# Performance work log

Measured on AMD Instinct MI355X. Metric: run time of the kernel, lower is better.

## Reference

```python
import jax, jax.numpy as jnp
import numpy as np
from jax.scipy.special import erf

FILTER_WIDTH = 23
NSIG = 20.0
PCT = 3.0  # normalization_percentile_threshold


def _gaussian_kernel(kernlen, nsig):
    # matches scipy-style: diff of normal CDF over linspace(-nsig, nsig)
    x = jnp.linspace(-nsig, nsig, kernlen + 1)
    cdf = 0.5 * (1.0 + erf(x / jnp.sqrt(2.0)))
    k1d = jnp.diff(cdf)
    k2d = jnp.outer(k1d, k1d)
    return (k2d / k2d.sum()).astype(jnp.float32)


def setup_inputs() -> dict:
    key = jax.random.key(0)
    k1, k2 = jax.random.split(key)
    N, C, H, W = 16, 3, 512, 512
    x = jax.random.uniform(k1, (N, C, H, W), dtype=jnp.float32)
    # binary circular-ish mask (fundus-style): random but mostly ones
    mask = (jax.random.uniform(k2, (N, 1, H, W)) > 0.1).astype(jnp.float32)
    kernel = _gaussian_kernel(FILTER_WIDTH, NSIG)
    return {"x": x, "mask": mask, "kernel": kernel}


def reference(x, mask, kernel):
    N, C, H, W = x.shape
    HW = H * W
    # --- median padding: torch.median returns the LOWER median -> sorted[(n-1)//2]
    med = jnp.sort(x.reshape(N, C, HW), axis=-1)[..., (HW - 1) // 2] + 0.2  # [N,C]
    x = mask * x + (1.0 - mask) * med[:, :, None, None]
    # --- get_hfc (Gaussian high-pass, depthwise blur with SAME padding)
    k = jnp.broadcast_to(kernel[None, None], (C, 1, kernel.shape[0], kernel.shape[1]))
    blur = jax.lax.conv_general_dilated(
        x, k, window_strides=(1, 1), padding="SAME",
        feature_group_count=C,
        dimension_numbers=("NCHW", "OIHW", "NCHW"))
    res = x - blur
    # --- quantize to 1/256 (torch .int() truncates toward zero) then per-(n,c)
    # percentile normalization; percentiles are computed on detached values
    temp = jnp.trunc(res * 256.0) / 256.0
    flat = temp.reshape(N, C, HW)
    lo = jnp.percentile(flat, PCT, axis=-1)[:, :, None, None]          # [N,C,1,1]
    hi = jnp.percentile(flat, 100.0 - PCT, axis=-1)[:, :, None, None]
    res = (res - lo) / (hi - lo)
    # --- sub_mask
    return res * mask
```

## Files before the change

### kernel.cpp

```cpp
#include <hip/hip_runtime.h>
#include <hip/hip_fp16.h>

#define W 512
#define H 512
#define HW (512*512)
#define NCH 3
#define MBINS 4096
#define PBINS 1024
#define MEDK ((HW-1)/2)
#define KW 23
#define KR 11

#define TR 32
#define TC 128
#define SR (TR + 2*KR)
#define SC (TC + 2*KR)
#define FSTR2 154
#define HSTR2 65
#define NQ 38
#define NSLOT (SR*NQ)
#define HBLK 16
#define CBLK 64
#define SENT 0x7C00u

typedef float f32x2 __attribute__((ext_vector_type(2)));

__global__ __launch_bounds__(256) void k_hist(const float* __restrict__ x,
                                              unsigned int* __restrict__ hist) {
    __shared__ unsigned int h[MBINS];
    int g = blockIdx.x >> 4;
    int chunk = blockIdx.x & 15;
    for (int i = threadIdx.x; i < MBINS; i += 256) h[i] = 0u;
    __syncthreads();
    const float4* xp = (const float4*)(x + (size_t)g*HW + (size_t)chunk*16384);
    #pragma unroll
    for (int hb = 0; hb < 2; ++hb) {
        float4 v[8];
        #pragma unroll
        for (int it = 0; it < 8; ++it) v[it] = xp[(hb*8 + it)*256 + threadIdx.x];
        #pragma unroll
        for (int it = 0; it < 8; ++it) {
            int b0 = min(MBINS-1, (int)(v[it].x * (float)MBINS));
            int b1 = min(MBINS-1, (int)(v[it].y * (float)MBINS));
            int b2 = min(MBINS-1, (int)(v[it].z * (float)MBINS));
            int b3 = min(MBINS-1, (int)(v[it].w * (float)MBINS));
            atomicAdd(&h[b0], 1u); atomicAdd(&h[b1], 1u);
            atomicAdd(&h[b2], 1u); atomicAdd(&h[b3], 1u);
        }
    }
    __syncthreads();
    unsigned int* gh = hist + (size_t)blockIdx.x*MBINS;
    for (int i = threadIdx.x; i < MBINS; i += 256) gh[i] = h[i];
}

__global__ __launch_bounds__(256) void k_medsel(const unsigned int* __restrict__ hist,
                                                const float* __restrict__ kern,
                                                float* __restrict__ s1d,
                                                float* __restrict__ med) {
    __shared__ unsigned int scan[256];
    const int g = blockIdx.x;
    const int tid = threadIdx.x;
    if (g == 0 && tid < KW) {
        float s = 0.f;
        for (int j = 0; j < KW; ++j) s += kern[tid*KW + j];
        s1d[tid] = s;
    }
    unsigned int local[16];
    #pragma unroll
    for (int i = 0; i < 16; ++i) local[i] = 0u;
    for (int c = 0; c < HBLK; ++c) {
        const uint4* p = (const uint4*)(hist + ((size_t)(g*HBLK + c))*MBINS + tid*16);
        #pragma unroll
        for (int q = 0; q < 4; ++q) {
            uint4 v = p[q];
            local[q*4+0] += v.x; local[q*4+1] += v.y;
            local[q*4+2] += v.z; local[q*4+3] += v.w;
        }
    }
    unsigned int s = 0;
    #pragma unroll
    for (int i = 0; i < 16; ++i) s += local[i];
    scan[tid] = s;
    __syncthreads();
    #pragma unroll
    for (int off = 1; off < 256; off <<= 1) {
        unsigned int t = (tid >= off) ? scan[tid - off] : 0u;
        __syncthreads();
        scan[tid] += t;
        __syncthreads();
    }
    unsigned int p = scan[tid] - s;
    if (p <= (unsigned)MEDK && (unsigned)MEDK < p + s) {
        unsigned int c = p;
        #pragma unroll
        for (int i = 0; i < 16; ++i) {
            if (c + local[i] > (unsigned)MEDK) {
                int bin = tid*16 + i;
                float frac = ((float)(MEDK - c) + 0.5f) / (float)local[i];
                med[g] = ((float)bin + frac) * (1.0f/(float)MBINS) + 0.2f;
                break;
            }
            c += local[i];
        }
    }
}

__device__ __forceinline__ void stage_slot(int slot, int r0, int c0, float medv,
                                           const float* __restrict__ xg,
                                           const float* __restrict__ mg,
                                           __half* __restrict__ fillh) {
    const int row = slot / NQ;
    const int q   = slot - row*NQ;
    const int gr  = r0 + row - KR;
    const int gc0q = c0 - 12 + q*4;
    const bool rowok = (unsigned)gr < (unsigned)H;
    float4 xv = {0.f,0.f,0.f,0.f}, mv = {0.f,0.f,0.f,0.f};
    if (rowok) {
        if (gc0q >= 0 && gc0q <= W-4) {
            xv = *(const float4*)(xg + gr*W + gc0q);
            mv = *(const float4*)(mg + gr*W + gc0q);
        } else {
            float* xe = (float*)&xv; float* me = (float*)&mv;
            #pragma unroll
            for (int e = 0; e < 4; ++e) {
                int gc = gc0q + e;
                if ((unsigned)gc < (unsigned)W) {
                    xe[e] = xg[gr*W + gc]; me[e] = mg[gr*W + gc];
                }
            }
        }
    }
    const float* xe = (const float*)&xv; const float* me = (const float*)&mv;
    #pragma unroll
    for (int e = 0; e < 4; ++e) {
        const int gc = gc0q + e;
        const int lc = gc - (c0 - KR);
        if (lc >= 0 && lc < SC) {
            float f = 0.f;
            if (rowok && (unsigned)gc < (unsigned)W)
                f = me[e]*xe[e] + (1.f - me[e])*medv;
            fillh[row*FSTR2 + lc] = __float2half(f);
        }
    }
}

__global__ __launch_bounds__(512) void k_conv(const float* __restrict__ x,
                                              const float* __restrict__ mask,
                                              const float* __restrict__ med,
                                              const float* __restrict__ s1d,
                                              unsigned short* __restrict__ res,
                                              unsigned int* __restrict__ phist) {
    __shared__ __half fillh[SR*FSTR2];
    __shared__ __half2 hbuf2[SR*HSTR2];
    __shared__ float sk[KW];
    __shared__ unsigned int h[PBINS];
    const int b   = blockIdx.x;
    const int g   = b >> 6;
    const int sub = b & 63;
    const int rb  = sub >> 2;
    const int cb  = sub & 3;
    const int r0  = rb*TR, c0 = cb*TC;
    const int n   = g / NCH;
    const int tid = threadIdx.x;
    for (int i = tid; i < PBINS; i += 512) h[i] = 0u;
    if (tid < KW) sk[tid] = s1d[tid];
    const float medv = med[g];
    const float* xg = x    + (size_t)g*HW;
    const float* mg = mask + (size_t)n*HW;

    {
        float4 xa[4], ma[4];
        #pragma unroll
        for (int s = 0; s < 4; ++s) {
            const int slot = tid + s*512;
            const int row = slot / NQ;
            const int q   = slot - row*NQ;
            const int gr  = r0 + row - KR;
            const int gc0q = c0 - 12 + q*4;
            const bool rowok = (unsigned)gr < (unsigned)H;
            float4 xv = {0.f,0.f,0.f,0.f}, mv = {0.f,0.f,0.f,0.f};
            if (rowok) {
                if (gc0q >= 0 && gc0q <= W-4) {
                    xv = *(const float4*)(xg + gr*W + gc0q);
                    mv = *(const float4*)(mg + gr*W + gc0q);
                } else {
                    float* xe = (float*)&xv; float* me = (float*)&mv;
                    #pragma unroll
                    for (int e = 0; e < 4; ++e) {
                        int gc = gc0q + e;
                        if ((unsigned)gc < (unsigned)W) {
                            xe[e] = xg[gr*W + gc]; me[e] = mg[gr*W + gc];
                        }
                    }
                }
            }
            xa[s] = xv; ma[s] = mv;
        }
        #pragma unroll
        for (int s = 0; s < 4; ++s) {
            const int slot = tid + s*512;
            const int row = slot / NQ;
            const int q   = slot - row*NQ;
            const int gr  = r0 + row - KR;
            const int gc0q = c0 - 12 + q*4;
            const bool rowok = (unsigned)gr < (unsigned)H;
            const float* xe = (const float*)&xa[s];
            const float* me = (const float*)&ma[s];
            #pragma unroll
            for (int e = 0; e < 4; ++e) {
                const int gc = gc0q + e;
                const int lc = gc - (c0 - KR);
                if (lc >= 0 && lc < SC) {
                    float f = 0.f;
                    if (rowok && (unsigned)gc < (unsigned)W)
                        f = me[e]*xe[e] + (1.f - me[e])*medv;
                    fillh[row*FSTR2 + lc] = __float2half(f);
                }
            }
        }
        if (tid < NSLOT - 2048)
            stage_slot(2048 + tid, r0, c0, medv, xg, mg, fillh);
    }
    __syncthreads();

    {
        const int row = tid & 63;
        const int cg  = tid >> 6;
        if (row < SR) {
            const __half2* fill2 = (const __half2*)fillh;
            #pragma unroll
            for (int half = 0; half < 2; ++half) {
                const int cg8 = cg + half*8;
                const int f2base = row*(FSTR2/2) + cg8*4;
                f32x2 acc[4] = {{0.f,0.f},{0.f,0.f},{0.f,0.f},{0.f,0.f}};
                #pragma unroll
                for (int t = 0; t < 15; ++t) {
                    const __half2 hp = fill2[f2base + t];
                    #pragma unroll
                    for (int u = 0; u < 2; ++u) {
                        const float v = u ? __high2float(hp) : __low2float(hp);
                        const int j = 2*t + u;
                        #pragma unroll
                        for (int p = 0; p < 4; ++p) {
                            const int d = j - 2*p;
                            if (d >= 1 && d <= 22) {
                                f32x2 kk = {sk[d], sk[d-1]};
                                acc[p] += kk * v;
                            } else if (d == 0) {
                                acc[p].x += sk[0]*v;
                            } else if (d == 23) {
                                acc[p].y += sk[22]*v;
                            }
                        }
                    }
                }
                #pragma unroll
                for (int p = 0; p < 4; ++p)
                    hbuf2[row*HSTR2 + cg8*4 + p] = __floats2half2_rn(acc[p].x, acc[p].y);
            }
        }
    }
    __syncthreads();

    {
        const int col = tid & 127;
        const int rg  = tid >> 7;
        const int lr0 = rg*8;
        const __half* hb = (const __half*)hbuf2;
        f32x2 acc[4] = {{0.f,0.f},{0.f,0.f},{0.f,0.f},{0.f,0.f}};
        #pragma unroll
        for (int j = 0; j < 30; ++j) {
            const float v = __half2float(hb[(lr0 + j)*(2*HSTR2) + col]);
            #pragma unroll
            for (int p = 0; p < 4; ++p) {
                const int d = j - 2*p;
                if (d >= 1 && d <= 22) {
                    f32x2 kk = {sk[d], sk[d-1]};
                    acc[p] += kk * v;
                } else if (d == 0) {
                    acc[p].x += sk[0]*v;
                } else if (d == 23) {
                    acc[p].y += sk[22]*v;
                }
            }
        }
        unsigned short* rout = res + (size_t)g*HW;
        #pragma unroll
        for (int o = 0; o < 8; ++o) {
            const float blur = (o & 1) ? acc[o>>1].y : acc[o>>1].x;
            const float fv = __half2float(fillh[(lr0 + o + KR)*FSTR2 + col + KR]);
            const float rv = fv - blur;
            const int r = r0 + lr0 + o;
            const float mv = mg[r*W + c0 + col];
            rout[r*W + c0 + col] =
                (mv != 0.f) ? __half_as_ushort(__float2half(rv)) : (unsigned short)SENT;
            int bin = (int)truncf(rv*256.f) + 512;
            bin = min(PBINS-1, max(0, bin));
            atomicAdd(&h[bin], 1u);
        }
    }
    __syncthreads();
    unsigned int* gh = phist + (size_t)b*PBINS;
    for (int i = tid; i < PBINS; i += 512) gh[i] = h[i];
}

__global__ __launch_bounds__(256) void k_pct(const unsigned int* __restrict__ phist,
                                             float* __restrict__ lohi) {
    __shared__ unsigned int scan[256];
    __shared__ float vsh[4];
    const int g = blockIdx.x;
    const int tid = threadIdx.x;
    unsigned int local[4];
    #pragma unroll
    for (int i = 0; i < 4; ++i) local[i] = 0u;
    for (int c = 0; c < CBLK; ++c) {
        uint4 v = *(const uint4*)(phist + ((size_t)(g*CBLK + c))*PBINS + tid*4);
        local[0] += v.x; local[1] += v.y; local[2] += v.z; local[3] += v.w;
    }
    unsigned int s = local[0] + local[1] + local[2] + local[3];
    scan[tid] = s;
    __syncthreads();
    #pragma unroll
    for (int off = 1; off < 256; off <<= 1) {
        unsigned int t = (tid >= off) ? scan[tid - off] : 0u;
        __syncthreads();
        scan[tid] += t;
        __syncthreads();
    }
    unsigned int p = scan[tid] - s;
    const double dl = (3.0/100.0)*(double)(HW-1);
    const double dh = (97.0/100.0)*(double)(HW-1);
    const long il = (long)dl, ih = (long)dh;
    const long ranks[4] = {il, il+1, ih, ih+1};
    #pragma unroll
    for (int ri = 0; ri < 4; ++ri) {
        long r = ranks[ri];
        if ((long)p <= r && r < (long)(p + s)) {
            unsigned int c = p;
            #pragma unroll
            for (int i = 0; i < 4; ++i) {
                if ((long)(c + local[i]) > r) {
                    vsh[ri] = (float)(tid*4 + i - 512) * (1.0f/256.0f);
                    break;
                }
                c += local[i];
            }
        }
    }
    __syncthreads();
    if (tid == 0) {
        double fl = dl - (double)il, fh = dh - (double)ih;
        double lo = (double)vsh[0] + fl*((double)vsh[1] - (double)vsh[0]);
        double hi = (double)vsh[2] + fh*((double)vsh[3] - (double)vsh[2]);
        lohi[2*g]   = (float)lo;
        lohi[2*g+1] = (float)hi;
    }
}

__global__ __launch_bounds__(256) void k_final(const unsigned short* __restrict__ res,
                                               const float* __restrict__ lohi,
                                               float* __restrict__ out) {
    size_t idx8 = (size_t)blockIdx.x*256 + threadIdx.x;
    size_t base = idx8*8;
    int g = (int)(base >> 18);
    float lo = lohi[2*g], hi = lohi[2*g+1];
    float inv = 1.0f/(hi - lo);
    uint4 rbits = *(const uint4*)(res + base);
    const unsigned short* u = (const unsigned short*)&rbits;
    float4 o0, o1;
    float* po0 = (float*)&o0;
    float* po1 = (float*)&o1;
    #pragma unroll
    for (int e = 0; e < 4; ++e)
        po0[e] = (u[e] == (unsigned short)SENT)
                   ? 0.f : (__half2float(__ushort_as_half(u[e])) - lo)*inv;
    #pragma unroll
    for (int e = 0; e < 4; ++e)
        po1[e] = (u[4+e] == (unsigned short)SENT)
                   ? 0.f : (__half2float(__ushort_as_half(u[4+e])) - lo)*inv;
    *(float4*)(out + base)     = o0;
    *(float4*)(out + base + 4) = o1;
}

extern "C" void kernel_launch(void* const* d_in, const int* in_sizes, int n_in,
                              void* d_out, int out_size, void* d_ws, size_t ws_size,
                              hipStream_t stream) {
    const float* x    = (const float*)d_in[0];
    const float* mask = (const float*)d_in[1];
    const float* kern = (const float*)d_in[2];
    float* out = (float*)d_out;

    char* ws = (char*)d_ws;
    unsigned int*   phist = (unsigned int*)ws;
    unsigned int*   mhist = (unsigned int*)(ws + 12582912);
    unsigned short* res16 = (unsigned short*)(ws + 25165824);
    float* med  = (float*)(ws + 50331648);
    float* s1d  = (float*)(ws + 50331904);
    float* lohi = (float*)(ws + 50332160);

    k_hist  <<<768,  256, 0, stream>>>(x, mhist);
    k_medsel<<<48,   256, 0, stream>>>(mhist, kern, s1d, med);
    k_conv  <<<3072, 512, 0, stream>>>(x, mask, med, s1d, res16, phist);
    k_pct   <<<48,   256, 0, stream>>>(phist, lohi);
    k_final <<<6144, 256, 0, stream>>>(res16, lohi, out);
}
```

Baseline: 183.8 us.

## Use fp16 dot2 for separable blur with transposed intermediate buffer

Rewrites both passes of the separable Gaussian blur to use packed fp16 dot2 instructions (v_dot2_f32_f16) with even/odd-shifted half2 kernel taps held in registers. The intermediate horizontal-blur buffer is stored transposed so the vertical pass can read contiguous half2 pairs. The histogram reduction loops in the median-select and percentile kernels are also batched to issue more loads before accumulating. This roughly halves the FMA instruction count but quantizes the kernel weights to fp16, which adds rounding error, and the transposed stores may cause LDS bank conflicts.

```diff
diff --git a/kernel.cpp b/kernel.cpp
--- a/kernel.cpp
+++ b/kernel.cpp
@@ -16,14 +16,45 @@
 #define SR (TR + 2*KR)
 #define SC (TC + 2*KR)
 #define FSTR2 154
-#define HSTR2 65
+#define TSTR 66
 #define NQ 38
 #define NSLOT (SR*NQ)
 #define HBLK 16
 #define CBLK 64
 #define SENT 0x7C00u
 
-typedef float f32x2 __attribute__((ext_vector_type(2)));
+typedef _Float16 h16x2 __attribute__((ext_vector_type(2)));
+
+static __device__ __forceinline__ float fdot2h(__half2 a, __half2 b, float c) {
+#if __has_builtin(__builtin_amdgcn_fdot2)
+    return __builtin_amdgcn_fdot2(__builtin_bit_cast(h16x2, a),
+                                  __builtin_bit_cast(h16x2, b), c, false);
+#else
+    return fmaf(__high2float(a), __high2float(b),
+           fmaf(__low2float(a),  __low2float(b),  c));
+#endif
+}
+
+static __device__ __forceinline__ void conv8_dot2(const __half2 (&w)[15],
+                                                  const __half2 (&eK)[11],
+                                                  const __half2 (&oK)[11],
+                                                  float sk0f, float sk22f,
+                                                  float (&out8)[8]) {
+    #pragma unroll
+    for (int k = 0; k < 8; k += 2) {
+        const int s = k >> 1;
+        float accE = 0.f, accO = 0.f;
+        #pragma unroll
+        for (int jj = 0; jj < 11; ++jj) {
+            accE = fdot2h(w[s+jj],   eK[jj], accE);
+            accO = fdot2h(w[s+1+jj], oK[jj], accO);
+        }
+        accE += sk22f * __low2float(w[s+11]);
+        accO += sk0f  * __high2float(w[s]);
+        out8[k]   = accE;
+        out8[k+1] = accO;
+    }
+}
 
 __global__ __launch_bounds__(256) void k_hist(const float* __restrict__ x,
                                               unsigned int* __restrict__ hist) {
@@ -68,13 +99,21 @@
     unsigned int local[16];
     #pragma unroll
     for (int i = 0; i < 16; ++i) local[i] = 0u;
-    for (int c = 0; c < HBLK; ++c) {
-        const uint4* p = (const uint4*)(hist + ((size_t)(g*HBLK + c))*MBINS + tid*16);
-        #pragma unroll
-        for (int q = 0; q < 4; ++q) {
-            uint4 v = p[q];
-            local[q*4+0] += v.x; local[q*4+1] += v.y;
-            local[q*4+2] += v.z; local[q*4+3] += v.w;
+    for (int c = 0; c < HBLK; c += 4) {
+        uint4 v[4][4];
+        #pragma unroll
+        for (int cc = 0; cc < 4; ++cc) {
+            const uint4* p = (const uint4*)(hist + ((size_t)(g*HBLK + c + cc))*MBINS + tid*16);
+            #pragma unroll
+            for (int q = 0; q < 4; ++q) v[cc][q] = p[q];
+        }
+        #pragma unroll
+        for (int cc = 0; cc < 4; ++cc) {
+            #pragma unroll
+            for (int q = 0; q < 4; ++q) {
+                local[q*4+0] += v[cc][q].x; local[q*4+1] += v[cc][q].y;
+                local[q*4+2] += v[cc][q].z; local[q*4+3] += v[cc][q].w;
+            }
         }
     }
     unsigned int s = 0;
@@ -151,8 +190,9 @@
                                               unsigned short* __restrict__ res,
                                               unsigned int* __restrict__ phist) {
     __shared__ __half fillh[SR*FSTR2];
-    __shared__ __half2 hbuf2[SR*HSTR2];
-    __shared__ float sk[KW];
+    __shared__ __half hbT[TC*TSTR];
+    __shared__ __half2 skE[11], skO[11];
+    __shared__ float sk0f_s, sk22f_s;
     __shared__ unsigned int h[PBINS];
     const int b   = blockIdx.x;
     const int g   = b >> 6;
@@ -163,7 +203,11 @@
     const int n   = g / NCH;
     const int tid = threadIdx.x;
     for (int i = tid; i < PBINS; i += 512) h[i] = 0u;
-    if (tid < KW) sk[tid] = s1d[tid];
+    if (tid < 11) {
+        skE[tid] = __floats2half2_rn(s1d[2*tid],   s1d[2*tid+1]);
+        skO[tid] = __floats2half2_rn(s1d[2*tid+1], s1d[2*tid+2]);
+    }
+    if (tid == 11) { sk0f_s = s1d[0]; sk22f_s = s1d[22]; }
     const float medv = med[g];
     const float* xg = x    + (size_t)g*HW;
     const float* mg = mask + (size_t)n*HW;
@@ -223,6 +267,11 @@
     }
     __syncthreads();
 
+    __half2 eK[11], oK[11];
+    #pragma unroll
+    for (int jj = 0; jj < 11; ++jj) { eK[jj] = skE[jj]; oK[jj] = skO[jj]; }
+    const float sk0f = sk0f_s, sk22f = sk22f_s;
+
     {
         const int row = tid & 63;
         const int cg  = tid >> 6;
@@ -231,32 +280,14 @@
             #pragma unroll
             for (int half = 0; half < 2; ++half) {
                 const int cg8 = cg + half*8;
-                const int f2base = row*(FSTR2/2) + cg8*4;
-                f32x2 acc[4] = {{0.f,0.f},{0.f,0.f},{0.f,0.f},{0.f,0.f}};
+                __half2 w[15];
                 #pragma unroll
-                for (int t = 0; t < 15; ++t) {
-                    const __half2 hp = fill2[f2base + t];
-                    #pragma unroll
-                    for (int u = 0; u < 2; ++u) {
-                        const float v = u ? __high2float(hp) : __low2float(hp);
-                        const int j = 2*t + u;
-                        #pragma unroll
-                        for (int p = 0; p < 4; ++p) {
-                            const int d = j - 2*p;
-                            if (d >= 1 && d <= 22) {
-                                f32x2 kk = {sk[d], sk[d-1]};
-                                acc[p] += kk * v;
-                            } else if (d == 0) {
-                                acc[p].x += sk[0]*v;
-                            } else if (d == 23) {
-                                acc[p].y += sk[22]*v;
-                            }
-                        }
-                    }
-                }
+                for (int t = 0; t < 15; ++t) w[t] = fill2[row*(FSTR2/2) + cg8*4 + t];
+                float out8[8];
+                conv8_dot2(w, eK, oK, sk0f, sk22f, out8);
                 #pragma unroll
-                for (int p = 0; p < 4; ++p)
-                    hbuf2[row*HSTR2 + cg8*4 + p] = __floats2half2_rn(acc[p].x, acc[p].y);
+                for (int k = 0; k < 8; ++k)
+                    hbT[(cg8*8 + k)*TSTR + row] = __float2half(out8[k]);
             }
         }
     }
@@ -266,30 +297,17 @@
         const int col = tid & 127;
         const int rg  = tid >> 7;
         const int lr0 = rg*8;
-        const __half* hb = (const __half*)hbuf2;
-        f32x2 acc[4] = {{0.f,0.f},{0.f,0.f},{0.f,0.f},{0.f,0.f}};
-        #pragma unroll
-        for (int j = 0; j < 30; ++j) {
-            const float v = __half2float(hb[(lr0 + j)*(2*HSTR2) + col]);
-            #pragma unroll
-            for (int p = 0; p < 4; ++p) {
-                const int d = j - 2*p;
-                if (d >= 1 && d <= 22) {
-                    f32x2 kk = {sk[d], sk[d-1]};
-                    acc[p] += kk * v;
-                } else if (d == 0) {
-                    acc[p].x += sk[0]*v;
-                } else if (d == 23) {
-                    acc[p].y += sk[22]*v;
-                }
-            }
-        }
+        const __half2* hb2 = (const __half2*)hbT;
+        __half2 w[15];
+        #pragma unroll
+        for (int t = 0; t < 15; ++t) w[t] = hb2[col*(TSTR/2) + (lr0 >> 1) + t];
+        float out8[8];
+        conv8_dot2(w, eK, oK, sk0f, sk22f, out8);
         unsigned short* rout = res + (size_t)g*HW;
         #pragma unroll
         for (int o = 0; o < 8; ++o) {
-            const float blur = (o & 1) ? acc[o>>1].y : acc[o>>1].x;
             const float fv = __half2float(fillh[(lr0 + o + KR)*FSTR2 + col + KR]);
-            const float rv = fv - blur;
+            const float rv = fv - out8[o];
             const int r = r0 + lr0 + o;
             const float mv = mg[r*W + c0 + col];
             rout[r*W + c0 + col] =
@@ -313,9 +331,16 @@
     unsigned int local[4];
     #pragma unroll
     for (int i = 0; i < 4; ++i) local[i] = 0u;
-    for (int c = 0; c < CBLK; ++c) {
-        uint4 v = *(const uint4*)(phist + ((size_t)(g*CBLK + c))*PBINS + tid*4);
-        local[0] += v.x; local[1] += v.y; local[2] += v.z; local[3] += v.w;
+    for (int c = 0; c < CBLK; c += 8) {
+        uint4 v[8];
+        #pragma unroll
+        for (int cc = 0; cc < 8; ++cc)
+            v[cc] = *(const uint4*)(phist + ((size_t)(g*CBLK + c + cc))*PBINS + tid*4);
+        #pragma unroll
+        for (int cc = 0; cc < 8; ++cc) {
+            local[0] += v[cc].x; local[1] += v[cc].y;
+            local[2] += v[cc].z; local[3] += v[cc].w;
+        }
     }
     unsigned int s = local[0] + local[1] + local[2] + local[3];
     scan[tid] = s;
```

New measurement: 174.0 us. 5.4% less time.
